# Kernel optimization log

Measured on AMD Instinct MI355X. Metric: run time of the kernel, lower is better.

Reference implementation:

```python
import jax, jax.numpy as jnp
import numpy as np

GAMMA = 0.25
GN_EPS = 1e-5


def setup_inputs() -> dict:
    key = jax.random.key(0)
    k1, k2, k3 = jax.random.split(key, 3)
    B, T, C = 16, 2048, 512
    G, V, Dv = 2, 320, 256
    x = jax.random.normal(k1, (B, T, C), dtype=jnp.float32)
    conv_w = jax.random.normal(k2, (G, C // G, C // G), dtype=jnp.float32) * 0.05
    gn_w = jnp.ones((C,), dtype=jnp.float32)
    gn_b = jnp.zeros((C,), dtype=jnp.float32)
    emb = 0.01 * jax.random.normal(k3, (V, G, Dv), dtype=jnp.float32)
    return {"x": x, "conv_w": conv_w, "gn_w": gn_w, "gn_b": gn_b, "emb": emb}


def _vq_forward(x, conv_w, gn_w, gn_b, emb):
    B, T, C = x.shape
    V, G, Dv = emb.shape
    sg = jax.lax.stop_gradient
    # time_first -> BxCxT
    xt = jnp.transpose(x, (0, 2, 1))  # [B,C,T]
    # grouped 1x1 conv (no bias)
    xg = xt.reshape(B, G, C // G, T)
    ze = jnp.einsum('goi,bgit->bgot', conv_w, xg)  # [B,G,C/G,T]
    # Fp32GroupNorm over (C/G, T) per group, biased variance
    zf = ze.astype(jnp.float32)
    mu = jnp.mean(zf, axis=(2, 3), keepdims=True)
    var = jnp.mean(jnp.square(zf - mu), axis=(2, 3), keepdims=True)
    zn = ((zf - mu) * jax.lax.rsqrt(var + GN_EPS)).reshape(B, C, T)
    ze = (zn * gn_w[None, :, None] + gn_b[None, :, None]).astype(ze.dtype)  # [B,C,T]
    # split into groups along feature dim: [B,T,G,Dv]
    ze_ = jnp.transpose(ze.reshape(B, G, Dv, T), (0, 3, 1, 2))
    # squared distances [V,B,T,G] (argmin of ||.||_2 == argmin of ||.||_2^2)
    d2 = (jnp.sum(jnp.square(ze_), axis=-1)[None]
          - 2.0 * jnp.einsum('btgd,vgd->vbtg', ze_, emb)
          + jnp.sum(jnp.square(emb), axis=-1)[:, None, None, :])
    idx = jnp.argmin(d2, axis=0)  # [B,T,G] int
    # gather nearest codewords per group
    zq = emb[idx, jnp.arange(G)[None, None, :]]  # [B,T,G,Dv]
    zq = jnp.transpose(zq.reshape(B, T, C), (0, 2, 1))  # [B,C,T]
    # straight-through
    out = sg(zq) + (ze - sg(ze))  # [B,C,T]
    # code perplexity (no grad)
    probs = jnp.mean(jax.nn.one_hot(sg(idx), V, dtype=jnp.float32), axis=(0, 1))  # [G,V]
    perplexity = jnp.sum(jnp.exp(-jnp.sum(probs * jnp.log(probs + 1e-7), axis=-1)))
    # losses
    zef, zqf = ze.astype(jnp.float32), zq.astype(jnp.float32)
    latent = jnp.mean(jnp.square(zqf - sg(zef)))
    commit = jnp.mean(jnp.square(zef - sg(zqf)))
    loss = latent + GAMMA * commit
    out = jnp.transpose(out, (0, 2, 1))  # back to BxTxC
    return out, loss, perplexity, idx


def reference(x, conv_w, gn_w, gn_b, emb):
    return _vq_forward(x, conv_w, gn_w, gn_b, emb)
```

## Files before the change

### kernel.cpp

```cpp
#include <hip/hip_runtime.h>

#define Bq 16
#define Tq 2048
#define Cq 512
#define Gq 2
#define CGq 256
#define Vq 320
#define Mq 32768
#define LOSS_OFF 16777216
#define PPL_OFF  16777217
#define IDX_OFF  16777218

#define MARGIN2 6.0e-3f
#define LIST_CAP 16384
#define LIST2_CAP 1024

#define WS_PCONV 0
#define WS_MU    8192
#define WS_RS    8320
#define WS_E2    8448
#define WS_S1    11008
#define WS_C1    13568
#define WS_LOSSF 16128
#define WS_CNT   16136
#define WS_CNT2  16140
#define WS_HIST  16144
#define WS_WSP   20480
#define WS_LISTQ 20480
#define WS_PLOSS 151552
#define WS_PL2   155648
#define WS_LIST2 172032
#define WS_Z2TAB 176128
#define WS_ESP   438272
#define WS_ZSP   806912


#define SL(X, r) ((X) * 16 + ((r) ^ ((X) & 7)))

#define WS_ESPH  806912
#define WS_ZSP2  1134592
#define WS_NEED  34689024ull

typedef short s16x8 __attribute__((ext_vector_type(8)));
typedef float f32x4v __attribute__((ext_vector_type(4)));

__device__ __forceinline__ unsigned rne16(float x) {
    unsigned u = __float_as_uint(x);
    return (u + 0x7fffu + ((u >> 16) & 1u)) >> 16;
}

__device__ __forceinline__ void bsplit3(float x, unsigned &h, unsigned &m, unsigned &l) {
    unsigned u = __float_as_uint(x);
    unsigned r1 = (u + 0x7fffu + ((u >> 16) & 1u)) & 0xffff0000u;
    h = r1 >> 16;
    float d1 = x - __uint_as_float(r1);
    unsigned u2 = __float_as_uint(d1);
    unsigned r2 = (u2 + 0x7fffu + ((u2 >> 16) & 1u)) & 0xffff0000u;
    m = r2 >> 16;
    float d2 = d1 - __uint_as_float(r2);
    unsigned u3 = __float_as_uint(d2);
    l = (u3 + 0x7fffu + ((u3 >> 16) & 1u)) >> 16;
}

__global__ __launch_bounds__(256) void k_prep(const float* __restrict__ w,
                                              const float* __restrict__ emb,
                                              const float* __restrict__ gw,
                                              const float* __restrict__ gb,
                                              unsigned char* __restrict__ wsp,
                                              unsigned char* __restrict__ esph,
                                              float* __restrict__ e2w,
                                              float* __restrict__ s1w,
                                              float* __restrict__ c1w) {
    int bx = blockIdx.x, tid = threadIdx.x;
    if (bx < 64) {
        int t = bx * 256 + tid;
        int g = t >> 13, o = (t >> 5) & 255, ihi = t & 31;
        const float* src = w + ((size_t)(g * 256 + o)) * 256 + ihi * 8;
        float xv[8];
        *(float4*)(xv + 0) = *(const float4*)(src);
        *(float4*)(xv + 4) = *(const float4*)(src + 4);
        unsigned ph[4] = {0,0,0,0}, pm[4] = {0,0,0,0}, pl[4] = {0,0,0,0};
#pragma unroll
        for (int e = 0; e < 8; e++) {
            unsigned h, m, l;
            bsplit3(xv[e], h, m, l);
            ph[e >> 1] |= h << ((e & 1) * 16);
            pm[e >> 1] |= m << ((e & 1) * 16);
            pl[e >> 1] |= l << ((e & 1) * 16);
        }
        int kc = ihi >> 2, quad = ihi & 3, ct = o >> 4, lf = o & 15;
        size_t base = (size_t)(g * 3) * 131072 + (size_t)kc * 16384 + ct * 1024 + quad * 256 + lf * 16;
        *(uint4*)(wsp + base + 0 * 131072) = *(uint4*)ph;
        *(uint4*)(wsp + base + 1 * 131072) = *(uint4*)pm;
        *(uint4*)(wsp + base + 2 * 131072) = *(uint4*)pl;
    } else if (bx < 224) {
        int row  = (bx - 64) * 4 + (tid >> 6);
        int lane = tid & 63;
        int g = row & 1;
        float4 v = *(const float4*)(emb + (size_t)row * 256 + lane * 4);
        float s = v.x * v.x + v.y * v.y + v.z * v.z + v.w * v.w;
        float4 g4 = *(const float4*)(gw + g * CGq + lane * 4);
        float4 b4 = *(const float4*)(gb + g * CGq + lane * 4);
        float c1 = g4.x * v.x + g4.y * v.y + g4.z * v.z + g4.w * v.w;
        float c2 = b4.x * v.x + b4.y * v.y + b4.z * v.z + b4.w * v.w;
#pragma unroll
        for (int m = 1; m < 64; m <<= 1) {
            s  += __shfl_xor(s, m);
            c1 += __shfl_xor(c1, m);
            c2 += __shfl_xor(c2, m);
        }
        if (lane == 0) {
            int idx = g * Vq + (row >> 1);
            e2w[idx] = s;
            s1w[idx] = s - 2.0f * c2;
            c1w[idx] = c1;
        }
    } else {
        int t = (bx - 224) * 256 + tid;
        int g  = t / 10240;
        int r  = t - g * 10240;
        int kc = r / 1280;
        int r2 = r - kc * 1280;
        int ct = r2 >> 6;
        int r3 = r2 & 63;
        int kq = r3 >> 4, l15 = r3 & 15;
        int v  = ct * 16 + l15;
        int k0 = kc * 32 + kq * 8;
        const float* src = emb + ((size_t)v * 2 + g) * 256 + k0;
        const float* gws = gw + g * CGq + k0;
        float xv[8], gv[8];
        *(float4*)(xv + 0) = *(const float4*)(src);
        *(float4*)(xv + 4) = *(const float4*)(src + 4);
        *(float4*)(gv + 0) = *(const float4*)(gws);
        *(float4*)(gv + 4) = *(const float4*)(gws + 4);
        unsigned ph[4] = {0,0,0,0};
#pragma unroll
        for (int e = 0; e < 8; e++) {
            unsigned h = rne16(xv[e] * gv[e]);
            ph[e >> 1] |= h << ((e & 1) * 16);
        }
        size_t base = (size_t)g * 163840 + (size_t)kc * 20480
                    + (size_t)((ct * 4 + kq) * 16 + l15) * 16;
        *(uint4*)(esph + base) = *(uint4*)ph;
    }
}

__global__ __launch_bounds__(256, 2) void k_convM(const float* __restrict__ x,
    const unsigned char* __restrict__ wsp, float* __restrict__ ze,
    double* __restrict__ pconv, unsigned char* __restrict__ zsp)
{
    __shared__ unsigned char lds[73728];
    __shared__ double reds[4], redq[4];
    uint4* Bs = (uint4*)lds;
    uint4* As = (uint4*)(lds + 49152);

    int tid = threadIdx.x, bx = blockIdx.x;
    int mt = bx >> 1, g = bx & 1;
    int m0 = mt * 128;
    int w = tid >> 6, lane = tid & 63;
    int quad = lane >> 4, l15 = lane & 15;
    int arow = tid >> 1, ah = tid & 1;
    int aw = arow >> 5, art = (arow >> 4) & 1, ar = arow & 15;
    const float* xrow = x + (size_t)(m0 + arow) * Cq + g * CGq + ah * 16;
    const unsigned char* wslab = wsp + (size_t)(g * 3) * 131072;

    f32x4v zero4 = {0.f, 0.f, 0.f, 0.f};
    f32x4v acc[2][16];
#pragma unroll
    for (int i = 0; i < 2; i++)
#pragma unroll
        for (int j = 0; j < 16; j++) acc[i][j] = zero4;

    for (int kc = 0; kc < 8; kc++) {
        if (kc) __syncthreads();
#pragma unroll
        for (int j = 0; j < 12; j++) {
            int L = (w * 12 + j) * 1024 + lane * 16;
            int p = L >> 14, r = L & 16383;
            __builtin_amdgcn_global_load_lds(
                (const __attribute__((address_space(1))) void*)(wslab + (size_t)p * 131072 + (size_t)kc * 16384 + r),
                (__attribute__((address_space(3))) void*)(lds + L), 16, 0, 0);
        }
        float xv[16];
        *(float4*)(xv + 0)  = *(const float4*)(xrow + kc * 32 + 0);
        *(float4*)(xv + 4)  = *(const float4*)(xrow + kc * 32 + 4);
        *(float4*)(xv + 8)  = *(const float4*)(xrow + kc * 32 + 8);
        *(float4*)(xv + 12) = *(const float4*)(xrow + kc * 32 + 12);
#pragma unroll
        for (int ii = 0; ii < 2; ii++) {
            unsigned ph[4] = {0,0,0,0}, pm[4] = {0,0,0,0}, pl[4] = {0,0,0,0};
#pragma unroll
            for (int e = 0; e < 8; e++) {
                unsigned h, m, l;
                bsplit3(xv[ii * 8 + e], h, m, l);
                ph[e >> 1] |= h << ((e & 1) * 16);
                pm[e >> 1] |= m << ((e & 1) * 16);
                pl[e >> 1] |= l << ((e & 1) * 16);
            }
            int aq = ah * 2 + ii;
            As[SL(((0 * 4 + aw) * 2 + art) * 4 + aq, ar)] = *(uint4*)ph;
            As[SL(((1 * 4 + aw) * 2 + art) * 4 + aq, ar)] = *(uint4*)pm;
            As[SL(((2 * 4 + aw) * 2 + art) * 4 + aq, ar)] = *(uint4*)pl;
        }
        __syncthreads();
        s16x8 afr[3][2];
#pragma unroll
        for (int p = 0; p < 3; p++)
#pragma unroll
            for (int rt = 0; rt < 2; rt++)
                afr[p][rt] = __builtin_bit_cast(s16x8,
                    As[SL(((p * 4 + w) * 2 + rt) * 4 + quad, l15)]);
#pragma unroll
        for (int ct = 0; ct < 16; ct++) {
            s16x8 b0 = __builtin_bit_cast(s16x8, Bs[0 * 1024 + ct * 64 + quad * 16 + l15]);
            s16x8 b1 = __builtin_bit_cast(s16x8, Bs[1 * 1024 + ct * 64 + quad * 16 + l15]);
            s16x8 b2 = __builtin_bit_cast(s16x8, Bs[2 * 1024 + ct * 64 + quad * 16 + l15]);
#pragma unroll
            for (int rt = 0; rt < 2; rt++) {
                acc[rt][ct] = __builtin_amdgcn_mfma_f32_16x16x32_bf16(afr[0][rt], b0, acc[rt][ct], 0, 0, 0);
                acc[rt][ct] = __builtin_amdgcn_mfma_f32_16x16x32_bf16(afr[1][rt], b0, acc[rt][ct], 0, 0, 0);
                acc[rt][ct] = __builtin_amdgcn_mfma_f32_16x16x32_bf16(afr[2][rt], b0, acc[rt][ct], 0, 0, 0);
                acc[rt][ct] = __builtin_amdgcn_mfma_f32_16x16x32_bf16(afr[0][rt], b1, acc[rt][ct], 0, 0, 0);
                acc[rt][ct] = __builtin_amdgcn_mfma_f32_16x16x32_bf16(afr[1][rt], b1, acc[rt][ct], 0, 0, 0);
                acc[rt][ct] = __builtin_amdgcn_mfma_f32_16x16x32_bf16(afr[0][rt], b2, acc[rt][ct], 0, 0, 0);
            }
        }
    }

    float s = 0.f, q = 0.f;
    float* zb = ze + (size_t)m0 * Cq + g * CGq;
#pragma unroll
    for (int rt = 0; rt < 2; rt++)
#pragma unroll
    for (int ct = 0; ct < 16; ct++)
#pragma unroll
    for (int j = 0; j < 4; j++) {
        float v = acc[rt][ct][j];
        zb[(size_t)(w * 32 + rt * 16 + quad * 4 + j) * Cq + ct * 16 + l15] = v;
        s += v;
        q = __builtin_fmaf(v, v, q);
    }
    double ds = (double)s, dq = (double)q;
#pragma unroll
    for (int m = 1; m < 64; m <<= 1) { ds += __shfl_xor(ds, m); dq += __shfl_xor(dq, m); }
    if (lane == 0) { reds[w] = ds; redq[w] = dq; }
    __syncthreads();
    if (tid == 0) {
        pconv[bx * 2 + 0] = reds[0] + reds[1] + reds[2] + reds[3];
        pconv[bx * 2 + 1] = redq[0] + redq[1] + redq[2] + redq[3];
    }

    {
        unsigned short* t16 = (unsigned short*)lds;
#pragma unroll
        for (int rt = 0; rt < 2; rt++)
#pragma unroll
        for (int ct = 0; ct < 16; ct++)
#pragma unroll
        for (int j = 0; j < 4; j++)
            t16[w * 8448 + (rt * 16 + quad * 4 + j) * 264 + ct * 16 + l15] =
                (unsigned short)rne16(acc[rt][ct][j]);
        __syncthreads();
        uint4* zt = (uint4*)(zsp + (size_t)bx * 65536);
        int rr = lane & 15, kq = lane >> 4;
#pragma unroll
        for (int kc8 = 0; kc8 < 8; kc8++)
#pragma unroll
        for (int rt = 0; rt < 2; rt++) {
            uint4 vf = *(uint4*)&t16[w * 8448 + (rt * 16 + rr) * 264 + kc8 * 32 + kq * 8];
            zt[((kc8 * 4 + w) * 2 + rt) * 64 + lane] = vf;
        }
    }
}

__global__ __launch_bounds__(256) void k_stats(const double* __restrict__ pconv,
                                               float* __restrict__ muw,
                                               float* __restrict__ rsw) {
    int tid = threadIdx.x;
    int bg = tid >> 3, r = tid & 7;
    int b = bg >> 1, g = bg & 1;
    double s = 0.0, q = 0.0;
    for (int j = r; j < 16; j += 8) {
        int pi = (b * 16 + j) * 2 + g;
        s += pconv[pi * 2 + 0];
        q += pconv[pi * 2 + 1];
    }
#pragma unroll
    for (int m = 1; m < 8; m <<= 1) { s += __shfl_xor(s, m); q += __shfl_xor(q, m); }
    if (r == 0) {
        double mu = s / 524288.0;
        double var = q / 524288.0 - mu * mu;
        double rs = 1.0 / sqrt(var + 1e-5);
        muw[bg] = (float)mu;
        rsw[bg] = (float)rs;
    }
}

__global__ __launch_bounds__(256) void k_z2(const float* __restrict__ ze,
    const float* __restrict__ gw, const float* __restrict__ gb,
    const float* __restrict__ muw, const float* __restrict__ rsw,
    float* __restrict__ z2tab)
{
    int tid = threadIdx.x, lane = tid & 63;
    int gwid = blockIdx.x * 4 + (tid >> 6);
    for (int rr = 0; rr < 16; rr++) {
        int q = gwid * 16 + rr;
        int m = q >> 1, g = q & 1;
        int bg = (m >> 11) * 2 + g;
        float muf = muw[bg], rsf = rsw[bg];
        float4 z  = *(const float4*)(ze + (size_t)m * Cq + g * CGq + lane * 4);
        float4 gv = *(const float4*)(gw + g * CGq + lane * 4);
        float4 bv = *(const float4*)(gb + g * CGq + lane * 4);
        float zn0 = (z.x - muf) * rsf * gv.x + bv.x;
        float zn1 = (z.y - muf) * rsf * gv.y + bv.y;
        float zn2 = (z.z - muf) * rsf * gv.z + bv.z;
        float zn3 = (z.w - muf) * rsf * gv.w + bv.w;
        float s = zn0 * zn0;
        s = __builtin_fmaf(zn1, zn1, s);
        s = __builtin_fmaf(zn2, zn2, s);
        s = __builtin_fmaf(zn3, zn3, s);
#pragma unroll
        for (int mm = 1; mm < 64; mm <<= 1) s += __shfl_xor(s, mm);
        if (lane == 0) z2tab[q] = s;
    }
}

__global__ __launch_bounds__(256, 2) void k_distA(const unsigned char* __restrict__ zsp,
    const unsigned char* __restrict__ esph,
    const float* __restrict__ muw, const float* __restrict__ rsw,
    const float* __restrict__ s1w, const float* __restrict__ c1w,
    const float* __restrict__ z2tab,
    float* dout,
    unsigned* __restrict__ cntw, unsigned* __restrict__ cnt2w,
    unsigned long long* __restrict__ listq, unsigned* __restrict__ list2,
    unsigned* __restrict__ hist, double* __restrict__ ploss)
{
    __shared__ unsigned char ldsA[16384];
    __shared__ unsigned char ldsB[40960];
    __shared__ float s0s[Vq];
    __shared__ double redp[4];

    int tid = threadIdx.x, bx = blockIdx.x;
    int mt = bx >> 1, g = bx & 1;
    int m0 = mt * 128;
    int bg = (m0 >> 11) * 2 + g;
    float muf = muw[bg], rsf = rsw[bg];
    float beta = 2.0f * rsf;
    float alpha = beta * muf;
    int w = tid >> 6, lane = tid & 63;
    int quad = lane >> 4, l15 = lane & 15;

    for (int i = tid; i < Vq; i += 256)
        s0s[i] = s1w[g * Vq + i] + alpha * c1w[g * Vq + i];

    const unsigned char* zt = zsp + (size_t)bx * 65536;
    const unsigned char* eslab = esph + (size_t)g * 163840;

#define STAGE_CHUNK(c, buf) do {                                                   \
    int Lw_ = w * 2048 + lane * 16;                                                \
    __builtin_amdgcn_global_load_lds(                                              \
        (const __attribute__((address_space(1))) void*)(zt + (size_t)(c) * 8192 + Lw_),          \
        (__attribute__((address_space(3))) void*)(ldsA + (buf) * 8192 + Lw_), 16, 0, 0);         \
    __builtin_amdgcn_global_load_lds(                                              \
        (const __attribute__((address_space(1))) void*)(zt + (size_t)(c) * 8192 + Lw_ + 1024),   \
        (__attribute__((address_space(3))) void*)(ldsA + (buf) * 8192 + Lw_ + 1024), 16, 0, 0);  \
    _Pragma("unroll")                                                              \
    for (int j_ = 0; j_ < 5; j_++) {                                               \
        int L_ = j_ * 4096 + tid * 16;                                             \
        __builtin_amdgcn_global_load_lds(                                          \
            (const __attribute__((address_space(1))) void*)(eslab + (size_t)(c) * 20480 + L_),   \
            (__attribute__((address_space(3))) void*)(ldsB + (buf) * 20480 + L_), 16, 0, 0);     \
    }                                                                              \
} while (0)

    f32x4v zero4 = {0.f, 0.f, 0.f, 0.f};
    f32x4v acc[2][20];
#pragma unroll
    for (int i = 0; i < 2; i++)
#pragma unroll
        for (int j = 0; j < 20; j++) acc[i][j] = zero4;

    STAGE_CHUNK(0, 0);
    __syncthreads();
    for (int kc8 = 0; kc8 < 8; kc8++) {
        int cur = kc8 & 1;
        if (kc8 < 7) STAGE_CHUNK(kc8 + 1, cur ^ 1);
        s16x8 afr0 = *(const s16x8*)(ldsA + cur * 8192 + (((w * 2 + 0) * 4 + quad) * 16 + l15) * 16);
        s16x8 afr1 = *(const s16x8*)(ldsA + cur * 8192 + (((w * 2 + 1) * 4 + quad) * 16 + l15) * 16);
#pragma unroll
        for (int ct = 0; ct < 20; ct++) {
            s16x8 b = *(const s16x8*)(ldsB + cur * 20480 + ((ct * 4 + quad) * 16 + l15) * 16);
            acc[0][ct] = __builtin_amdgcn_mfma_f32_16x16x32_bf16(afr0, b, acc[0][ct], 0, 0, 0);
            acc[1][ct] = __builtin_amdgcn_mfma_f32_16x16x32_bf16(afr1, b, acc[1][ct], 0, 0, 0);
        }
        __syncthreads();
    }
#undef STAGE_CHUNK

    double lacc = 0.0;
#pragma unroll
    for (int rt = 0; rt < 2; rt++)
#pragma unroll
    for (int j = 0; j < 4; j++) {
        float m1 = 3.402823466e+38f; int i1 = 0;
#pragma unroll
        for (int ct = 0; ct < 20; ct++) {
            float d2a = s0s[ct * 16 + l15] - beta * acc[rt][ct][j];
            if (d2a < m1) { m1 = d2a; i1 = ct * 16 + l15; }
        }
#pragma unroll
        for (int mm = 1; mm < 16; mm <<= 1) {
            float ov = __shfl_xor(m1, mm);
            int   oi = __shfl_xor(i1, mm);
            if (ov < m1 || (ov == m1 && oi < i1)) { m1 = ov; i1 = oi; }
        }
        float thr = m1 + MARGIN2;
        unsigned mask = 0;
#pragma unroll
        for (int ct = 0; ct < 20; ct++) {
            float d2a = s0s[ct * 16 + l15] - beta * acc[rt][ct][j];
            if (d2a <= thr) mask |= (1u << ct);
        }
        int cnt = __popc(mask);
#pragma unroll
        for (int mm = 1; mm < 16; mm <<= 1) cnt += __shfl_xor(cnt, mm);
        int mrow = m0 + w * 32 + rt * 16 + quad * 4 + j;
        unsigned q = (unsigned)mrow * 2u + (unsigned)g;
        unsigned flag = 0;
        if (cnt > 1) {
            if ((i1 & 15) == l15) mask &= ~(1u << (i1 >> 4));
            int cl2 = __popc(mask);
            int inc = cl2;
#pragma unroll
            for (int off = 1; off < 16; off <<= 1) {
                int t = __shfl_up(inc, off, 16);
                if (l15 >= off) inc += t;
            }
            int pre = inc - cl2;
            if (cnt <= 5) {
                int pos_ = 0;
                if (l15 == 0) pos_ = (int)atomicAdd(cntw, 1u);
                pos_ = __shfl(pos_, 0, 16);
                if ((unsigned)pos_ < LIST_CAP) {
                    flag = 512u;
                    unsigned long long contrib = 0ull;
                    unsigned mm2 = mask; int k = pre;
                    while (mm2) {
                        int ct2 = __ffs(mm2) - 1; mm2 &= mm2 - 1;
                        contrib |= ((unsigned long long)(unsigned)(ct2 * 16 + l15)) << (20 + 9 * k);
                        k++;
                    }
#pragma unroll
                    for (int mm = 1; mm < 16; mm <<= 1)
                        contrib |= __shfl_xor(contrib, mm);
                    if (l15 == 0)
                        listq[pos_] = (unsigned long long)q
                                    | ((unsigned long long)(unsigned)cnt << 17) | contrib;
                }
            } else {
                if (l15 == 0) {
                    unsigned p2 = atomicAdd(cnt2w, 1u);
                    if (p2 < LIST2_CAP) { list2[p2] = q; flag = 512u; }
                }
            }
        }
        if (l15 == 0) {
            if (flag) {
                dout[IDX_OFF + q] = __uint_as_float((unsigned)i1 | flag);
            } else {
                dout[IDX_OFF + q] = (float)i1;
                atomicAdd(&hist[g * Vq + i1], 1u);
                lacc += (double)z2tab[q] + (double)m1;
            }
        }
    }
#pragma unroll
    for (int mm = 1; mm < 64; mm <<= 1) lacc += __shfl_xor(lacc, mm);
    if (lane == 0) redp[w] = lacc;
    __syncthreads();
    if (tid == 0) ploss[bx] = redp[0] + redp[1] + redp[2] + redp[3];
}

__global__ __launch_bounds__(256) void k_exF(const float* __restrict__ emb,
    const float* __restrict__ gw, const float* __restrict__ gb,
    const float* __restrict__ muw, const float* __restrict__ rsw,
    const float* __restrict__ e2w, float* dout,
    unsigned* __restrict__ hist, double* __restrict__ ploss2,
    const unsigned long long* __restrict__ listq, const unsigned* __restrict__ cntw,
    double* __restrict__ lossf,
    const unsigned* __restrict__ cnt2w, const unsigned* __restrict__ list2)
{
    int tid = threadIdx.x, lane = tid & 63;
    int gwid = blockIdx.x * 4 + (tid >> 6);
    int cslot = lane >> 2, j = lane & 3;
    unsigned nn = *cntw; if (nn > LIST_CAP) nn = LIST_CAP;
    int n = (int)nn;
    double lacc = 0.0;
    for (int it = gwid; it < n; it += 2048) {
        unsigned long long e = listq[it];
        unsigned q = (unsigned)(e & 0x1FFFFull);
        int cnt = (int)((e >> 17) & 7u);
        int m = (int)(q >> 1), g = (int)(q & 1u);
        int bg = (m >> 11) * 2 + g;
        float muf = muw[bg], rsf = rsw[bg];
        int v = (int)(__float_as_uint(dout[IDX_OFF + q]) & 511u);
        if (cslot >= 1 && cslot < cnt)
            v = (int)((e >> (20 + 9 * (cslot - 1))) & 511ull);
        const float* zb  = dout + (size_t)m * Cq + g * CGq;
        const float* gwb = gw + g * CGq;
        const float* gbb = gb + g * CGq;
        const float* eb  = emb + ((size_t)v * Gq + g) * CGq;
        float z2p = 0.f, dp = 0.f;
        for (int kc = 0; kc < 16; kc++) {
            int k0 = kc * 16 + j * 4;
            float4 z  = *(const float4*)(zb + k0);
            float4 gv = *(const float4*)(gwb + k0);
            float4 bv = *(const float4*)(gbb + k0);
            float4 e4 = *(const float4*)(eb + k0);
            float zn0 = __fadd_rn(__fmul_rn(__fmul_rn(__fsub_rn(z.x, muf), rsf), gv.x), bv.x);
            float zn1 = __fadd_rn(__fmul_rn(__fmul_rn(__fsub_rn(z.y, muf), rsf), gv.y), bv.y);
            float zn2 = __fadd_rn(__fmul_rn(__fmul_rn(__fsub_rn(z.z, muf), rsf), gv.z), bv.z);
            float zn3 = __fadd_rn(__fmul_rn(__fmul_rn(__fsub_rn(z.w, muf), rsf), gv.w), bv.w);
            z2p = __builtin_fmaf(zn0, zn0, z2p);
            z2p = __builtin_fmaf(zn1, zn1, z2p);
            z2p = __builtin_fmaf(zn2, zn2, z2p);
            z2p = __builtin_fmaf(zn3, zn3, z2p);
            dp = __builtin_fmaf(zn0, e4.x, dp);
            dp = __builtin_fmaf(zn1, e4.y, dp);
            dp = __builtin_fmaf(zn2, e4.z, dp);
            dp = __builtin_fmaf(zn3, e4.w, dp);
        }
        z2p += __shfl_xor(z2p, 1); z2p += __shfl_xor(z2p, 2);
        dp  += __shfl_xor(dp, 1);  dp  += __shfl_xor(dp, 2);
        float d2 = __fadd_rn(__fsub_rn(z2p, 2.0f * dp), e2w[g * Vq + v]);
#pragma unroll
        for (int mm = 4; mm < 64; mm <<= 1) {
            float od = __shfl_xor(d2, mm);
            int   ov = __shfl_xor(v, mm);
            if (od < d2 || (od == d2 && ov < v)) { d2 = od; v = ov; }
        }
        if (lane == 0) {
            dout[IDX_OFF + q] = (float)v;
            atomicAdd(&hist[g * Vq + v], 1u);
            lacc += (double)d2;
        }
    }
    if (lane == 0) ploss2[gwid] = lacc;

    unsigned nn2 = *cnt2w; if (nn2 > LIST2_CAP) nn2 = LIST2_CAP;
    int n2 = (int)nn2;
    for (int it = gwid; it < n2; it += 2048) {
        int q = (int)list2[it];
        int m = q >> 1, g = q & 1;
        int bg = (m >> 11) * 2 + g;
        float muf = muw[bg], rsf = rsw[bg];
        const float* zb = dout + (size_t)m * Cq + g * CGq;
        int k0 = lane * 4;
        float4 z  = *(const float4*)(zb + k0);
        float4 gv = *(const float4*)(gw + g * CGq + k0);
        float4 bv = *(const float4*)(gb + g * CGq + k0);
        float zn0 = __fadd_rn(__fmul_rn(__fmul_rn(__fsub_rn(z.x, muf), rsf), gv.x), bv.x);
        float zn1 = __fadd_rn(__fmul_rn(__fmul_rn(__fsub_rn(z.y, muf), rsf), gv.y), bv.y);
        float zn2 = __fadd_rn(__fmul_rn(__fmul_rn(__fsub_rn(z.z, muf), rsf), gv.z), bv.z);
        float zn3 = __fadd_rn(__fmul_rn(__fmul_rn(__fsub_rn(z.w, muf), rsf), gv.w), bv.w);
        float s = 0.f;
        for (int kc = 0; kc < 16; kc++) {
            int src = (lane & 3) + kc * 4;
            float a0 = __shfl(zn0, src), a1 = __shfl(zn1, src);
            float a2 = __shfl(zn2, src), a3 = __shfl(zn3, src);
            s = __builtin_fmaf(a0, a0, s);
            s = __builtin_fmaf(a1, a1, s);
            s = __builtin_fmaf(a2, a2, s);
            s = __builtin_fmaf(a3, a3, s);
        }
        s += __shfl_xor(s, 1); s += __shfl_xor(s, 2);
        float z2 = s;
        float m1 = 3.402823466e+38f; int i1 = 0;
        for (int v = 0; v < Vq; v += 2) {
            const float* e0 = emb + ((size_t)v * Gq + g) * CGq + k0;
            float4 ea = *(const float4*)e0;
            float4 eb4 = *(const float4*)(e0 + Gq * CGq);
            float da = zn0 * ea.x;  da = __builtin_fmaf(zn1, ea.y, da);
            da = __builtin_fmaf(zn2, ea.z, da); da = __builtin_fmaf(zn3, ea.w, da);
            float db = zn0 * eb4.x; db = __builtin_fmaf(zn1, eb4.y, db);
            db = __builtin_fmaf(zn2, eb4.z, db); db = __builtin_fmaf(zn3, eb4.w, db);
#pragma unroll
            for (int mm = 1; mm < 64; mm <<= 1) { da += __shfl_xor(da, mm); db += __shfl_xor(db, mm); }
            float d2a = __fadd_rn(__fsub_rn(z2, 2.0f * da), e2w[g * Vq + v]);
            float d2b = __fadd_rn(__fsub_rn(z2, 2.0f * db), e2w[g * Vq + v + 1]);
            if (d2a < m1) { m1 = d2a; i1 = v; }
            if (d2b < m1) { m1 = d2b; i1 = v + 1; }
        }
        if (lane == 0) {
            dout[IDX_OFF + q] = (float)i1;
            atomicAdd(&hist[g * Vq + i1], 1u);
            atomicAdd(lossf, (double)m1);
        }
    }
}

__global__ __launch_bounds__(256) void k_out(const float* __restrict__ emb, float* dout) {
    size_t u = (size_t)blockIdx.x * 256 + threadIdx.x;
    size_t pos = u * 4;
    int m = (int)(pos >> 9);
    int c = (int)(pos & 511);
    int g = c >> 8, d = c & 255;
    int v = (int)dout[IDX_OFF + (size_t)m * Gq + g];
    float4 o = *(const float4*)(emb + ((size_t)(v * 2 + g)) * 256 + d);
    *(float4*)(dout + pos) = o;
}

__global__ __launch_bounds__(256) void k_final(const double* __restrict__ ploss,
                                               const double* __restrict__ ploss2,
                                               const double* __restrict__ lossf,
                                               const unsigned* __restrict__ hist,
                                               float* dout) {
    __shared__ double redl[4], red0[4], red1[4];
    int tid = threadIdx.x;
    double s = 0.0;
    for (int i = tid; i < 512; i += 256) s += ploss[i];
    for (int i = tid; i < 2048; i += 256) s += ploss2[i];
#pragma unroll
    for (int m = 1; m < 64; m <<= 1) s += __shfl_xor(s, m);
    double e0 = 0.0, e1 = 0.0;
    for (int pid = tid; pid < 640; pid += 256) {
        double p = (double)hist[pid] * (1.0 / 32768.0);
        double t = p * log(p + 1e-7);
        if (pid < 320) e0 += t; else e1 += t;
    }
#pragma unroll
    for (int m = 1; m < 64; m <<= 1) { e0 += __shfl_xor(e0, m); e1 += __shfl_xor(e1, m); }
    int lane = tid & 63, wv_ = tid >> 6;
    if (lane == 0) { redl[wv_] = s; red0[wv_] = e0; red1[wv_] = e1; }
    __syncthreads();
    if (tid == 0) {
        double S  = redl[0] + redl[1] + redl[2] + redl[3] + *lossf;
        double E0 = red0[0] + red0[1] + red0[2] + red0[3];
        double E1 = red1[0] + red1[1] + red1[2] + red1[3];
        dout[LOSS_OFF] = (float)(1.25 * S / 16777216.0);
        dout[PPL_OFF]  = (float)(exp(-E0) + exp(-E1));
    }
}

extern "C" void kernel_launch(void* const* d_in, const int* in_sizes, int n_in,
                              void* d_out, int out_size, void* d_ws, size_t ws_size,
                              hipStream_t stream) {
    const float* x   = (const float*)d_in[0];
    const float* w   = (const float*)d_in[1];
    const float* gw  = (const float*)d_in[2];
    const float* gb  = (const float*)d_in[3];
    const float* emb = (const float*)d_in[4];
    float* dout = (float*)d_out;
    char* ws = (char*)d_ws;
    double* pconv   = (double*)(ws + WS_PCONV);
    float* muw      = (float*)(ws + WS_MU);
    float* rsw      = (float*)(ws + WS_RS);
    float* e2w      = (float*)(ws + WS_E2);
    float* s1w      = (float*)(ws + WS_S1);
    float* c1w      = (float*)(ws + WS_C1);
    double* lossf   = (double*)(ws + WS_LOSSF);
    unsigned* cntw  = (unsigned*)(ws + WS_CNT);
    unsigned* cnt2w = (unsigned*)(ws + WS_CNT2);
    unsigned* hist  = (unsigned*)(ws + WS_HIST);
    unsigned char* wsp = (unsigned char*)(ws + WS_WSP);
    unsigned long long* listq = (unsigned long long*)(ws + WS_LISTQ);
    double* ploss   = (double*)(ws + WS_PLOSS);
    double* ploss2  = (double*)(ws + WS_PL2);
    unsigned* list2 = (unsigned*)(ws + WS_LIST2);
    float* z2tab    = (float*)(ws + WS_Z2TAB);
    unsigned char* esph = (unsigned char*)(ws + WS_ESPH);
    unsigned char* zsp  = (unsigned char*)(ws + WS_ZSP2);

    hipMemsetAsync(ws + WS_LOSSF, 0, 2576, stream);
    k_prep<<<304, 256, 0, stream>>>(w, emb, gw, gb, wsp, esph, e2w, s1w, c1w);
    k_convM<<<512, 256, 0, stream>>>(x, wsp, dout, pconv, zsp);
    k_stats<<<1, 256, 0, stream>>>(pconv, muw, rsw);
    k_z2<<<1024, 256, 0, stream>>>(dout, gw, gb, muw, rsw, z2tab);
    k_distA<<<512, 256, 0, stream>>>(zsp, esph, muw, rsw, s1w, c1w, z2tab, dout,
                                     cntw, cnt2w, listq, list2, hist, ploss);
    k_exF<<<512, 256, 0, stream>>>(emb, gw, gb, muw, rsw, e2w, dout, hist, ploss2,
                                   listq, cntw, lossf, cnt2w, list2);
    k_out<<<16384, 256, 0, stream>>>(emb, dout);
    k_final<<<1, 256, 0, stream>>>(ploss, ploss2, lossf, hist, dout);
}
```

Baseline: 194.2 us.

## Load MFMA operands directly from global memory instead of LDS double-buffering

The distance GEMM kernel now drops its LDS staging buffers and async global-to-LDS double buffering. Each wave reads its A fragments and all 20 B fragments straight from global memory into registers before issuing the MFMAs. This removes per-chunk barriers and LDS traffic, and the smaller shared footprint may allow more blocks per CU. In exchange every wave re-reads the shared codebook slab from global/L2 with no reuse through LDS, register pressure rises, and there is no explicit prefetch to hide latency.

```diff
diff --git a/kernel.cpp b/kernel.cpp
--- a/kernel.cpp
+++ b/kernel.cpp
@@ -31,15 +31,10 @@
 #define WS_PL2   155648
 #define WS_LIST2 172032
 #define WS_Z2TAB 176128
-#define WS_ESP   438272
-#define WS_ZSP   806912
-
-
-#define SL(X, r) ((X) * 16 + ((r) ^ ((X) & 7)))
-
 #define WS_ESPH  806912
 #define WS_ZSP2  1134592
-#define WS_NEED  34689024ull
+
+#define SL(X, r) ((X) * 16 + ((r) ^ ((X) & 7)))
 
 typedef short s16x8 __attribute__((ext_vector_type(8)));
 typedef float f32x4v __attribute__((ext_vector_type(4)));
@@ -335,8 +330,6 @@
     unsigned long long* __restrict__ listq, unsigned* __restrict__ list2,
     unsigned* __restrict__ hist, double* __restrict__ ploss)
 {
-    __shared__ unsigned char ldsA[16384];
-    __shared__ unsigned char ldsB[40960];
     __shared__ float s0s[Vq];
     __shared__ double redp[4];
 
@@ -352,26 +345,10 @@
 
     for (int i = tid; i < Vq; i += 256)
         s0s[i] = s1w[g * Vq + i] + alpha * c1w[g * Vq + i];
-
-    const unsigned char* zt = zsp + (size_t)bx * 65536;
-    const unsigned char* eslab = esph + (size_t)g * 163840;
-
-#define STAGE_CHUNK(c, buf) do {                                                   \
-    int Lw_ = w * 2048 + lane * 16;                                                \
-    __builtin_amdgcn_global_load_lds(                                              \
-        (const __attribute__((address_space(1))) void*)(zt + (size_t)(c) * 8192 + Lw_),          \
-        (__attribute__((address_space(3))) void*)(ldsA + (buf) * 8192 + Lw_), 16, 0, 0);         \
-    __builtin_amdgcn_global_load_lds(                                              \
-        (const __attribute__((address_space(1))) void*)(zt + (size_t)(c) * 8192 + Lw_ + 1024),   \
-        (__attribute__((address_space(3))) void*)(ldsA + (buf) * 8192 + Lw_ + 1024), 16, 0, 0);  \
-    _Pragma("unroll")                                                              \
-    for (int j_ = 0; j_ < 5; j_++) {                                               \
-        int L_ = j_ * 4096 + tid * 16;                                             \
-        __builtin_amdgcn_global_load_lds(                                          \
-            (const __attribute__((address_space(1))) void*)(eslab + (size_t)(c) * 20480 + L_),   \
-            (__attribute__((address_space(3))) void*)(ldsB + (buf) * 20480 + L_), 16, 0, 0);     \
-    }                                                                              \
-} while (0)
+    __syncthreads();
+
+    const uint4* zt    = (const uint4*)(zsp + (size_t)bx * 65536);
+    const uint4* ebase = (const uint4*)(esph + (size_t)g * 163840);
 
     f32x4v zero4 = {0.f, 0.f, 0.f, 0.f};
     f32x4v acc[2][20];
@@ -380,22 +357,20 @@
 #pragma unroll
         for (int j = 0; j < 20; j++) acc[i][j] = zero4;
 
-    STAGE_CHUNK(0, 0);
-    __syncthreads();
     for (int kc8 = 0; kc8 < 8; kc8++) {
-        int cur = kc8 & 1;
-        if (kc8 < 7) STAGE_CHUNK(kc8 + 1, cur ^ 1);
-        s16x8 afr0 = *(const s16x8*)(ldsA + cur * 8192 + (((w * 2 + 0) * 4 + quad) * 16 + l15) * 16);
-        s16x8 afr1 = *(const s16x8*)(ldsA + cur * 8192 + (((w * 2 + 1) * 4 + quad) * 16 + l15) * 16);
+        s16x8 a0 = __builtin_bit_cast(s16x8, zt[(kc8 * 4 + w) * 128 + lane]);
+        s16x8 a1 = __builtin_bit_cast(s16x8, zt[(kc8 * 4 + w) * 128 + 64 + lane]);
+        s16x8 bfr[20];
+#pragma unroll
+        for (int ct = 0; ct < 20; ct++)
+            bfr[ct] = __builtin_bit_cast(s16x8,
+                ebase[kc8 * 1280 + (ct * 4 + quad) * 16 + l15]);
 #pragma unroll
         for (int ct = 0; ct < 20; ct++) {
-            s16x8 b = *(const s16x8*)(ldsB + cur * 20480 + ((ct * 4 + quad) * 16 + l15) * 16);
-            acc[0][ct] = __builtin_amdgcn_mfma_f32_16x16x32_bf16(afr0, b, acc[0][ct], 0, 0, 0);
-            acc[1][ct] = __builtin_amdgcn_mfma_f32_16x16x32_bf16(afr1, b, acc[1][ct], 0, 0, 0);
-        }
-        __syncthreads();
-    }
-#undef STAGE_CHUNK
+            acc[0][ct] = __builtin_amdgcn_mfma_f32_16x16x32_bf16(a0, bfr[ct], acc[0][ct], 0, 0, 0);
+            acc[1][ct] = __builtin_amdgcn_mfma_f32_16x16x32_bf16(a1, bfr[ct], acc[1][ct], 0, 0, 0);
+        }
+    }
 
     double lacc = 0.0;
 #pragma unroll
```

Measured after the change: 205.4 us. 5.8% more time.
